# Optimization experiments

Measured on AMD Instinct MI355X. Metric: run time of the kernel, lower is better.

The kernel has to match this reference:

```python
import jax, jax.numpy as jnp
import numpy as np
import math

N_NODES = 100000
N_EDGES = 1600000
CUTOFF = 6.0          # max_radius
NUM_RBF = 128         # ExpNormalSmearing num_rbf
GAUSS_MIN, GAUSS_MAX, GAUSS_NB = 0.0, 10.0, 32  # GaussianExpansion(0, 10, 32)


def setup_inputs() -> dict:
    key = jax.random.key(0)
    k1, k2 = jax.random.split(key)
    pos = jax.random.normal(k1, (N_NODES, 3), dtype=jnp.float32)
    edge_index = jax.random.randint(k2, (2, N_EDGES), 0, N_NODES, dtype=jnp.int64)
    return {"pos": pos, "edge_index": edge_index}


def _cosine_cutoff(d):
    # CosineCutoff with cutoff_lower=0
    c = 0.5 * (jnp.cos(d * (math.pi / CUTOFF)) + 1.0)
    return c * (d < CUTOFF).astype(d.dtype)


def _expnormal_smearing(d):
    # ExpNormalSmearing(cutoff_lower=0, cutoff_upper=CUTOFF, num_rbf=NUM_RBF)
    alpha = 5.0 / CUTOFF
    start = math.exp(-CUTOFF)
    means = jnp.linspace(start, 1.0, NUM_RBF, dtype=jnp.float32)
    beta = (2.0 / NUM_RBF * (1.0 - start)) ** (-2)
    d = d[:, None]                                   # [E,1]
    return _cosine_cutoff(d) * jnp.exp(-beta * (jnp.exp(-alpha * d) - means) ** 2)


def _gaussian_expansion(d):
    # GaussianExpansion(0, 10, 32)
    centers = jnp.linspace(GAUSS_MIN, GAUSS_MAX, GAUSS_NB, dtype=jnp.float32)
    width = 0.5 * (GAUSS_MAX - GAUSS_MIN) / GAUSS_NB
    d = d[:, None]
    return jnp.exp(-((d - centers) ** 2) / (2.0 * width * width))


def reference(pos, edge_index):
    src = edge_index[0]
    dst = edge_index[1]
    vec = pos[src] - pos[dst]                        # [E,3] irregular gather
    dist = jnp.sqrt(jnp.sum(vec * vec, axis=-1) + 1e-12)  # [E]
    exp_feat = _expnormal_smearing(dist)             # [E,128]
    gauss_feat = _gaussian_expansion(dist)           # [E,32]
    return jnp.concatenate([exp_feat, gauss_feat], axis=-1)  # [E,160]
```

## Files before the change

### kernel.cpp

```cpp
#include <hip/hip_runtime.h>
#include <math.h>

#define N_NODES   100000
#define N_EDGES   1600000
#define NUM_RBF   128
#define NUM_GAUSS 32
#define NFEAT     160
#define CUTOFF    6.0f

#define EPB    64
#define BLOCK  256

__global__ __launch_bounds__(BLOCK) void edge_feat_kernel(
    const float* __restrict__ pos,
    const int*   __restrict__ eidx,
    float*       __restrict__ out)
{
    __shared__ float s_d[EPB];
    __shared__ float s_c[EPB];
    __shared__ float s_t[EPB];

    const int blockEdge0 = blockIdx.x * EPB;
    const int tid = threadIdx.x;

    if (tid < EPB) {
        const int e = blockEdge0 + tid;
        const int s = eidx[e];
        const int t = eidx[N_EDGES + e];
        const float dx = pos[3*s + 0] - pos[3*t + 0];
        const float dy = pos[3*s + 1] - pos[3*t + 1];
        const float dz = pos[3*s + 2] - pos[3*t + 2];
        const float dist = sqrtf(dx*dx + dy*dy + dz*dz + 1e-12f);
        s_d[tid] = dist;
        const float c = 0.5f * (__cosf(dist * (float)(M_PI / 6.0)) + 1.0f);
        s_c[tid] = (dist < CUTOFF) ? c : 0.0f;
        s_t[tid] = __expf(-(5.0f / 6.0f) * dist);
    }
    __syncthreads();

    const float start = (float)0.0024787521766663585;
    const float mstep = (float)((1.0 - 0.0024787521766663585) / (NUM_RBF - 1));
    const float beta  = (float)(1.0 /
        ((2.0 / NUM_RBF * (1.0 - 0.0024787521766663585)) *
         (2.0 / NUM_RBF * (1.0 - 0.0024787521766663585))));
    const float gstep = (float)(10.0 / (NUM_GAUSS - 1));
    const float ginv  = 20.48f;

    float4* out4 = (float4*)(out + (size_t)blockEdge0 * NFEAT);
    const int n4 = EPB * NFEAT / 4;
    for (int i = tid; i < n4; i += BLOCK) {
        const int f4 = i * 4;
        const int e  = i / 40;
        const int f  = f4 - e * NFEAT;
        const float d = s_d[e];
        float4 r;
        if (f < NUM_RBF) {
            const float c = s_c[e];
            const float t = s_t[e];
            #pragma unroll
            for (int j = 0; j < 4; ++j) {
                const float m = start + (float)(f + j) * mstep;
                const float u = t - m;
                ((float*)&r)[j] = c * __expf(-beta * u * u);
            }
        } else {
            const int g = f - NUM_RBF;
            #pragma unroll
            for (int j = 0; j < 4; ++j) {
                const float ctr = (float)(g + j) * gstep;
                const float u = d - ctr;
                ((float*)&r)[j] = __expf(-ginv * u * u);
            }
        }
        out4[i] = r;
    }
}

extern "C" void kernel_launch(void* const* d_in, const int* in_sizes, int n_in,
                              void* d_out, int out_size, void* d_ws, size_t ws_size,
                              hipStream_t stream) {
    const float* pos  = (const float*)d_in[0];
    const int*   eidx = (const int*)d_in[1];
    float*       out  = (float*)d_out;

    const int nblocks = N_EDGES / EPB;
    edge_feat_kernel<<<nblocks, BLOCK, 0, stream>>>(pos, eidx, out);
}
```

Before: 1.000 ms.

## Assign fixed feature columns per thread and fold exponent scale into exp2

```diff
diff --git a/kernel.cpp b/kernel.cpp
--- a/kernel.cpp
+++ b/kernel.cpp
@@ -9,16 +9,25 @@
 #define CUTOFF    6.0f
 
 #define EPB    64
-#define BLOCK  256
+#define BLOCK  320
+#define COLS   40
+#define EPI    (BLOCK/COLS)
+#define NITER  (EPB/EPI)
+
+static __device__ __forceinline__ float fast_exp2(float x) {
+#if __has_builtin(__builtin_amdgcn_exp2f)
+    return __builtin_amdgcn_exp2f(x);
+#else
+    return __expf(0.6931471805599453f * x);
+#endif
+}
 
 __global__ __launch_bounds__(BLOCK) void edge_feat_kernel(
     const float* __restrict__ pos,
     const int*   __restrict__ eidx,
     float*       __restrict__ out)
 {
-    __shared__ float s_d[EPB];
-    __shared__ float s_c[EPB];
-    __shared__ float s_t[EPB];
+    __shared__ float4 s_edge[EPB];
 
     const int blockEdge0 = blockIdx.x * EPB;
     const int tid = threadIdx.x;
@@ -31,12 +40,16 @@
         const float dy = pos[3*s + 1] - pos[3*t + 1];
         const float dz = pos[3*s + 2] - pos[3*t + 2];
         const float dist = sqrtf(dx*dx + dy*dy + dz*dz + 1e-12f);
-        s_d[tid] = dist;
         const float c = 0.5f * (__cosf(dist * (float)(M_PI / 6.0)) + 1.0f);
-        s_c[tid] = (dist < CUTOFF) ? c : 0.0f;
-        s_t[tid] = __expf(-(5.0f / 6.0f) * dist);
+        const float cc = (dist < CUTOFF) ? c : 0.0f;
+        const float te = __expf(-(5.0f / 6.0f) * dist);
+        s_edge[tid] = make_float4(dist, cc, te, 0.0f);
     }
     __syncthreads();
+
+    const int col   = tid % COLS;
+    const int eiter = tid / COLS;
+    const bool isRBF = (col < NUM_RBF / 4);
 
     const float start = (float)0.0024787521766663585;
     const float mstep = (float)((1.0 - 0.0024787521766663585) / (NUM_RBF - 1));
@@ -45,34 +58,44 @@
          (2.0 / NUM_RBF * (1.0 - 0.0024787521766663585))));
     const float gstep = (float)(10.0 / (NUM_GAUSS - 1));
     const float ginv  = 20.48f;
+    const float LOG2E = 1.4426950408889634f;
+
+    const int f0 = col * 4;
+    float4 C;
+    float SB;
+    if (isRBF) {
+        C.x = start + (float)(f0 + 0) * mstep;
+        C.y = start + (float)(f0 + 1) * mstep;
+        C.z = start + (float)(f0 + 2) * mstep;
+        C.w = start + (float)(f0 + 3) * mstep;
+        SB  = sqrtf(beta * LOG2E);
+    } else {
+        const int g0 = f0 - NUM_RBF;
+        C.x = (float)(g0 + 0) * gstep;
+        C.y = (float)(g0 + 1) * gstep;
+        C.z = (float)(g0 + 2) * gstep;
+        C.w = (float)(g0 + 3) * gstep;
+        SB  = sqrtf(ginv * LOG2E);
+    }
 
     float4* out4 = (float4*)(out + (size_t)blockEdge0 * NFEAT);
-    const int n4 = EPB * NFEAT / 4;
-    for (int i = tid; i < n4; i += BLOCK) {
-        const int f4 = i * 4;
-        const int e  = i / 40;
-        const int f  = f4 - e * NFEAT;
-        const float d = s_d[e];
+    #pragma unroll
+    for (int k = 0; k < NITER; ++k) {
+        const float4 es = s_edge[k * EPI + eiter];
+        const float X = isRBF ? es.z : es.x;
+        const float A = isRBF ? es.y : 1.0f;
         float4 r;
-        if (f < NUM_RBF) {
-            const float c = s_c[e];
-            const float t = s_t[e];
-            #pragma unroll
-            for (int j = 0; j < 4; ++j) {
-                const float m = start + (float)(f + j) * mstep;
-                const float u = t - m;
-                ((float*)&r)[j] = c * __expf(-beta * u * u);
-            }
-        } else {
-            const int g = f - NUM_RBF;
-            #pragma unroll
-            for (int j = 0; j < 4; ++j) {
-                const float ctr = (float)(g + j) * gstep;
-                const float u = d - ctr;
-                ((float*)&r)[j] = __expf(-ginv * u * u);
-            }
+        {
+            const float vx = (X - C.x) * SB;
+            const float vy = (X - C.y) * SB;
+            const float vz = (X - C.z) * SB;
+            const float vw = (X - C.w) * SB;
+            r.x = A * fast_exp2(-vx * vx);
+            r.y = A * fast_exp2(-vy * vy);
+            r.z = A * fast_exp2(-vz * vz);
+            r.w = A * fast_exp2(-vw * vw);
         }
-        out4[i] = r;
+        out4[k * BLOCK + tid] = r;
     }
 }
 
```

Result: no change. 988.5 us (-1.2%).
